# Kernel optimization log

Measured on AMD Instinct MI355X. Metric: run time of the kernel, lower is better.

The kernel has to match this reference:

```python
import jax, jax.numpy as jnp
import numpy as np

EMBED = 1024  # scale uses channel (= embed_size), faithful to original


def setup_inputs() -> dict:
    key = jax.random.key(0)
    k1, k2, k3, k4 = jax.random.split(key, 4)
    B, S, E, H = 4, 4096, EMBED, 64
    x = jax.random.normal(k1, (B, S, E), dtype=jnp.float32)
    Wk = jax.random.normal(k2, (E, H), dtype=jnp.float32) * (E ** -0.5)
    Wq = jax.random.normal(k3, (E, H), dtype=jnp.float32) * (E ** -0.5)
    Wv = jax.random.normal(k4, (E, H), dtype=jnp.float32) * (E ** -0.5)
    return {"x": x, "Wk": Wk, "Wq": Wq, "Wv": Wv}


def reference(x, Wk, Wq, Wv):
    # x: [B,S,E]; Wk/Wq/Wv: [E,H]
    B, S, E = x.shape
    k = jnp.einsum('bse,eh->bsh', x, Wk)
    q = jnp.einsum('bse,eh->bsh', x, Wq)
    v = jnp.einsum('bse,eh->bsh', x, Wv)
    # NOTE: original scales by channel**-0.5 (embed dim), not head_size
    scores = jnp.einsum('bqh,bkh->bqk', q, k) * (E ** -0.5)
    causal = jnp.tril(jnp.ones((S, S), dtype=bool))
    scores = jnp.where(causal, scores, -jnp.inf)
    attn = jax.nn.softmax(scores, axis=-1)
    # dropout treated as identity (eval mode) for deterministic reference
    out = jnp.einsum('bqk,bkh->bqh', attn, v)
    return out
```

## Files before the change

### kernel.cpp

```cpp
#include <hip/hip_runtime.h>
#include <hip/hip_bf16.h>
#include <math.h>

#define BATCH 4
#define SEQ   4096
#define EMB   1024
#define HD    64
#define SCALE 0.03125f
#define NSTRIPE 4

typedef __attribute__((ext_vector_type(8))) short short8;
typedef __attribute__((ext_vector_type(4))) float f32x4;

__device__ __forceinline__ short8 ld8g(const __hip_bfloat16* p) {
    union { uint4 u; short8 s; } cv;
    cv.u = *(const uint4*)p;
    return cv.s;
}
__device__ __forceinline__ short8 ld8l(const void* p) {
    union { uint4 u; short8 s; } cv;
    cv.u = *(const uint4*)p;
    return cv.s;
}
__device__ __forceinline__ unsigned short bfb(float a) {
    union { __hip_bfloat16 h; unsigned short u; } cv;
    cv.h = __hip_bfloat16(a);
    return cv.u;
}

__device__ __forceinline__ void gld16(const void* g, const void* lds_base) {
    __builtin_amdgcn_global_load_lds(
        (const __attribute__((address_space(1))) void*)(unsigned long long)(uintptr_t)g,
        (__attribute__((address_space(3))) void*)(unsigned)(uintptr_t)lds_base,
        16, 0, 0);
}

__global__ __launch_bounds__(256) void prep_w(
    const float* __restrict__ Wk, const float* __restrict__ Wq,
    const float* __restrict__ Wv, __hip_bfloat16* __restrict__ WT)
{
    __shared__ float ls[64][65];
    const int wsel = blockIdx.x >> 4;
    const int kblk = blockIdx.x & 15;
    const int k0   = kblk * 64;
    const float* W = (wsel == 0) ? Wq : (wsel == 1) ? Wk : Wv;
    const int t = threadIdx.x;
#pragma unroll
    for (int i = 0; i < 4; ++i) {
        const int idx = t + i * 256;
        const int row = idx >> 4;
        const int c4  = idx & 15;
        const float4 v = *(const float4*)(W + (size_t)(k0 + row) * HD + c4 * 4);
        ls[row][c4 * 4 + 0] = v.x; ls[row][c4 * 4 + 1] = v.y;
        ls[row][c4 * 4 + 2] = v.z; ls[row][c4 * 4 + 3] = v.w;
    }
    __syncthreads();
    const int h   = t >> 2;
    const int kk0 = (t & 3) * 16;
#pragma unroll
    for (int i = 0; i < 2; ++i) {
        const int kk = kk0 + i * 8;
        union { unsigned short u[8]; uint4 q; } pk;
#pragma unroll
        for (int j = 0; j < 8; ++j) pk.u[j] = bfb(ls[kk + j][h]);
        *(uint4*)(WT + (size_t)(wsel * 64 + h) * EMB + k0 + kk) = pk.q;
    }
}

__global__ __launch_bounds__(256) void gemm_proj(
    const float* __restrict__ x,
    const __hip_bfloat16* __restrict__ WT,
    __hip_bfloat16* __restrict__ qs,
    __hip_bfloat16* __restrict__ kb,
    __hip_bfloat16* __restrict__ vT)
{
    __shared__ __align__(16) char sm[8 * 1040 + 24 * 1040];
    char* smA = sm;
    char* smB = sm + 8 * 1040;

    const int tid  = threadIdx.x;
    const int lane = tid & 63;
    const int c    = lane & 15;
    const int quad = lane >> 4;
    const int w    = tid >> 6;
    const int rw   = w & 1;
    const int nh   = w >> 1;
    const int R0   = blockIdx.x * 32;

    const int rrA = lane >> 4;
    const int ciA = (lane & 15) ^ (rrA << 1);
    const int rrB = lane >> 3;
    const int ciB = (lane & 7) ^ rrB;

    const int rA  = rw * 16 + c;
    const int gA  = rA >> 2;
    const int rrr = rA & 3;
    const char* paBase = smA + gA * 1040 + rrr * 256;

    f32x4 acc[6];
#pragma unroll
    for (int f = 0; f < 6; ++f) acc[f] = (f32x4){0.f, 0.f, 0.f, 0.f};

    for (int s = 0; s < 16; ++s) {
        const int k0 = s * 64;
#pragma unroll
        for (int j = 0; j < 2; ++j) {
            const int g = w * 2 + j;
            const float* ga = x + (size_t)(R0 + g * 4 + rrA) * EMB + k0 + ciA * 4;
            gld16(ga, smA + g * 1040);
        }
#pragma unroll
        for (int j = 0; j < 6; ++j) {
            const int gb = w * 6 + j;
            const __hip_bfloat16* gw = WT + (size_t)(gb * 8 + rrB) * EMB + k0 + ciB * 8;
            gld16(gw, smB + gb * 1040);
        }
        __syncthreads();

#pragma unroll
        for (int ks = 0; ks < 2; ++ks) {
            const int ci0 = ks * 8 + quad * 2;
            const int ps0 = ci0 ^ (rrr << 1);
            const char* pa = paBase + ps0 * 16;
            const float4 fa = *(const float4*)pa;
            const float4 fb = *(const float4*)(pa + 16);
            union { unsigned short u[8]; short8 s8; } av;
            av.u[0] = bfb(fa.x); av.u[1] = bfb(fa.y);
            av.u[2] = bfb(fa.z); av.u[3] = bfb(fa.w);
            av.u[4] = bfb(fb.x); av.u[5] = bfb(fb.y);
            av.u[6] = bfb(fb.z); av.u[7] = bfb(fb.w);
#pragma unroll
            for (int f = 0; f < 6; ++f) {
                const int n   = nh * 96 + f * 16 + c;
                const int gB  = n >> 3;
                const int rB  = n & 7;
                const int psb = (ks * 4 + quad) ^ rB;
                const short8 bfrag = ld8l(smB + gB * 1040 + rB * 128 + psb * 16);
                acc[f] = __builtin_amdgcn_mfma_f32_16x16x32_bf16(av.s8, bfrag, acc[f], 0, 0, 0);
            }
        }
        __syncthreads();
    }

#pragma unroll
    for (int f = 0; f < 6; ++f) {
#pragma unroll
        for (int r = 0; r < 4; ++r) {
            const int m = R0 + rw * 16 + quad * 4 + r;
            const int n = nh * 96 + f * 16 + c;
            const float val = acc[f][r];
            if (n < 64) {
                qs[(size_t)m * HD + n] = __hip_bfloat16(val * SCALE);
            } else if (n < 128) {
                kb[(size_t)m * HD + (n - 64)] = __hip_bfloat16(val);
            } else {
                const int b  = m >> 12;
                const int sq = m & (SEQ - 1);
                const int sp = (sq & ~63) | ((sq & 15) << 2) | ((sq >> 4) & 3);
                vT[((size_t)b * HD + (n - 128)) * SEQ + sp] = __hip_bfloat16(val);
            }
        }
    }
}

__global__ __launch_bounds__(256) void attn_kernel(
    const __hip_bfloat16* __restrict__ qs,
    const __hip_bfloat16* __restrict__ kmat,
    const __hip_bfloat16* __restrict__ vT,
    float* __restrict__ outacc,
    float* __restrict__ lacc)
{
    __shared__ __align__(16) char smK[64 * 128];
    __shared__ __align__(16) char smV[64 * 128];
    __shared__ unsigned int Ps[4][16 * 36];

    const int tid  = threadIdx.x;
    const int w    = tid >> 6;
    const int lane = tid & 63;
    const int c    = lane & 15;
    const int quad = lane >> 4;

    const int g      = blockIdx.x;
    const int gen    = g >> 8;
    const int jj     = g & 255;
    const int b      = jj & 3;
    const int r_     = jj >> 2;
    const int t      = (gen & 1) ? r_ : 63 - r_;
    const int stripe = gen;
    const int q0w    = t * 64 + w * 16;

    const __hip_bfloat16* kbb = kmat + (size_t)b * SEQ * HD;
    const __hip_bfloat16* vTb = vT + (size_t)b * HD * SEQ;

    const __hip_bfloat16* qp = qs + ((size_t)b * SEQ + q0w + c) * HD + quad * 8;
    const short8 aq0 = ld8g(qp);
    const short8 aq1 = ld8g(qp + 32);

    const int rr = lane >> 3;
    const int ci = (lane & 7) ^ rr;

    f32x4 o0 = {0.f,0.f,0.f,0.f}, o1 = o0, o2 = o0, o3 = o0;
    f32x4 lp = {0.f,0.f,0.f,0.f};
    const f32x4 z = {0.f,0.f,0.f,0.f};

    for (int T = stripe; T <= t; T += NSTRIPE) {
        const int k0 = T << 6;

#pragma unroll
        for (int j = 0; j < 2; ++j) {
            const int grp = w * 2 + j;
            const int row = grp * 8 + rr;
            gld16(kbb + (size_t)(k0 + row) * HD + ci * 8, smK + grp * 1024);
            gld16(vTb + (size_t)row * SEQ + k0 + ci * 8, smV + grp * 1024);
        }
        __syncthreads();

        f32x4 sf[4];
#pragma unroll
        for (int f = 0; f < 4; ++f) {
            const int kr = f * 16 + c;
            const char* kp = smK + kr * 128;
            const short8 bk0 = ld8l(kp + ((quad    ) ^ (kr & 7)) * 16);
            const short8 bk1 = ld8l(kp + ((quad + 4) ^ (kr & 7)) * 16);
            sf[f] = __builtin_amdgcn_mfma_f32_16x16x32_bf16(aq0, bk0, z, 0, 0, 0);
            sf[f] = __builtin_amdgcn_mfma_f32_16x16x32_bf16(aq1, bk1, sf[f], 0, 0, 0);
        }

        if (T == t) {
#pragma unroll
            for (int f = 0; f < 4; ++f) {
                const int key = k0 + f * 16 + c;
#pragma unroll
                for (int r = 0; r < 4; ++r)
                    if (key > q0w + quad * 4 + r) sf[f][r] = -1e30f;
            }
        }

        float p[4][4];
#pragma unroll
        for (int f = 0; f < 4; ++f)
#pragma unroll
            for (int r = 0; r < 4; ++r)
                p[f][r] = __expf(sf[f][r]);
#pragma unroll
        for (int r = 0; r < 4; ++r) {
            lp[r] += (p[0][r] + p[1][r]) + (p[2][r] + p[3][r]);
            uint2 dd;
            dd.x = (unsigned int)bfb(p[0][r]) | ((unsigned int)bfb(p[1][r]) << 16);
            dd.y = (unsigned int)bfb(p[2][r]) | ((unsigned int)bfb(p[3][r]) << 16);
            *(uint2*)&Ps[w][(quad * 4 + r) * 36 + c * 2] = dd;
        }

        const short8 ap0 = ld8l(&Ps[w][c * 36 + quad * 4]);
        const short8 ap1 = ld8l(&Ps[w][c * 36 + 16 + quad * 4]);

        {
            const int vr = 0 * 16 + c;
            const char* vp = smV + vr * 128;
            const short8 bv0 = ld8l(vp + ((quad    ) ^ (vr & 7)) * 16);
            const short8 bv1 = ld8l(vp + ((quad + 4) ^ (vr & 7)) * 16);
            o0 = __builtin_amdgcn_mfma_f32_16x16x32_bf16(ap0, bv0, o0, 0, 0, 0);
            o0 = __builtin_amdgcn_mfma_f32_16x16x32_bf16(ap1, bv1, o0, 0, 0, 0);
        }
        {
            const int vr = 1 * 16 + c;
            const char* vp = smV + vr * 128;
            const short8 bv0 = ld8l(vp + ((quad    ) ^ (vr & 7)) * 16);
            const short8 bv1 = ld8l(vp + ((quad + 4) ^ (vr & 7)) * 16);
            o1 = __builtin_amdgcn_mfma_f32_16x16x32_bf16(ap0, bv0, o1, 0, 0, 0);
            o1 = __builtin_amdgcn_mfma_f32_16x16x32_bf16(ap1, bv1, o1, 0, 0, 0);
        }
        {
            const int vr = 2 * 16 + c;
            const char* vp = smV + vr * 128;
            const short8 bv0 = ld8l(vp + ((quad    ) ^ (vr & 7)) * 16);
            const short8 bv1 = ld8l(vp + ((quad + 4) ^ (vr & 7)) * 16);
            o2 = __builtin_amdgcn_mfma_f32_16x16x32_bf16(ap0, bv0, o2, 0, 0, 0);
            o2 = __builtin_amdgcn_mfma_f32_16x16x32_bf16(ap1, bv1, o2, 0, 0, 0);
        }
        {
            const int vr = 3 * 16 + c;
            const char* vp = smV + vr * 128;
            const short8 bv0 = ld8l(vp + ((quad    ) ^ (vr & 7)) * 16);
            const short8 bv1 = ld8l(vp + ((quad + 4) ^ (vr & 7)) * 16);
            o3 = __builtin_amdgcn_mfma_f32_16x16x32_bf16(ap0, bv0, o3, 0, 0, 0);
            o3 = __builtin_amdgcn_mfma_f32_16x16x32_bf16(ap1, bv1, o3, 0, 0, 0);
        }
        __syncthreads();
    }

#pragma unroll
    for (int r = 0; r < 4; ++r) {
        float v = lp[r];
        v += __shfl_xor(v, 1, 64);
        v += __shfl_xor(v, 2, 64);
        v += __shfl_xor(v, 4, 64);
        v += __shfl_xor(v, 8, 64);
        lp[r] = v;
    }

    float* ob = outacc + ((size_t)b * SEQ + q0w) * HD;
#pragma unroll
    for (int r = 0; r < 4; ++r) {
        const int row = quad * 4 + r;
        atomicAdd(&ob[row * HD +  0 + c], o0[r]);
        atomicAdd(&ob[row * HD + 16 + c], o1[r]);
        atomicAdd(&ob[row * HD + 32 + c], o2[r]);
        atomicAdd(&ob[row * HD + 48 + c], o3[r]);
        if (c == 0) atomicAdd(&lacc[(size_t)b * SEQ + q0w + row], lp[r]);
    }
}

__global__ __launch_bounds__(256) void normalize_kernel(
    float* __restrict__ out, const float* __restrict__ lacc)
{
    const int idx = blockIdx.x * 256 + threadIdx.x;
    out[idx] /= lacc[idx >> 6];
}

extern "C" void kernel_launch(void* const* d_in, const int* in_sizes, int n_in,
                              void* d_out, int out_size, void* d_ws, size_t ws_size,
                              hipStream_t stream)
{
    (void)in_sizes; (void)n_in; (void)out_size; (void)ws_size;
    const float* x  = (const float*)d_in[0];
    const float* Wk = (const float*)d_in[1];
    const float* Wq = (const float*)d_in[2];
    const float* Wv = (const float*)d_in[3];
    float* out = (float*)d_out;

    const size_t BSH = (size_t)BATCH * SEQ * HD;
    __hip_bfloat16* qs = (__hip_bfloat16*)d_ws;
    __hip_bfloat16* kb = qs + BSH;
    __hip_bfloat16* vT = kb + BSH;
    __hip_bfloat16* WT = vT + BSH;
    float* lacc = (float*)(WT + 192 * EMB);

    prep_w<<<48, 256, 0, stream>>>(Wk, Wq, Wv, WT);
    gemm_proj<<<BATCH * SEQ / 32, 256, 0, stream>>>(x, WT, qs, kb, vT);
    hipMemsetAsync(out, 0, BSH * sizeof(float), stream);
    hipMemsetAsync(lacc, 0, (size_t)BATCH * SEQ * sizeof(float), stream);
    attn_kernel<<<NSTRIPE * BATCH * (SEQ / 64), 256, 0, stream>>>(qs, kb, vT, out, lacc);
    normalize_kernel<<<BATCH * SEQ * HD / 256, 256, 0, stream>>>(out, lacc);
}
```

Baseline: 148.2 us.

## Double-buffer projection GEMM and replace atomic split-K reduction with partial buffers

The projection GEMM now uses two shared-memory stages so the next K-tile's global-to-LDS loads are issued before computing the current tile, with one barrier per iteration. The attention kernel writes per-stripe partial outputs and row sums to separate workspace slices instead of using float atomics. A vectorized normalize kernel then sums the stripes and divides, which removes the two memsets. This trades atomic traffic and the memsets for more workspace and extra reads in the normalize pass, and doubles the GEMM's LDS footprint.

```diff
diff --git a/kernel.cpp b/kernel.cpp
--- a/kernel.cpp
+++ b/kernel.cpp
@@ -74,9 +74,7 @@
     __hip_bfloat16* __restrict__ kb,
     __hip_bfloat16* __restrict__ vT)
 {
-    __shared__ __align__(16) char sm[8 * 1040 + 24 * 1040];
-    char* smA = sm;
-    char* smB = sm + 8 * 1040;
+    __shared__ __align__(16) char sm[2][8 * 1040 + 24 * 1040];
 
     const int tid  = threadIdx.x;
     const int lane = tid & 63;
@@ -95,28 +93,39 @@
     const int rA  = rw * 16 + c;
     const int gA  = rA >> 2;
     const int rrr = rA & 3;
-    const char* paBase = smA + gA * 1040 + rrr * 256;
 
     f32x4 acc[6];
 #pragma unroll
     for (int f = 0; f < 6; ++f) acc[f] = (f32x4){0.f, 0.f, 0.f, 0.f};
 
+#define STAGE(buf, kk)                                                          \
+    do {                                                                        \
+        char* sA = sm[buf];                                                     \
+        char* sB = sm[buf] + 8 * 1040;                                          \
+        _Pragma("unroll")                                                       \
+        for (int j = 0; j < 2; ++j) {                                           \
+            const int g = w * 2 + j;                                            \
+            gld16(x + (size_t)(R0 + g * 4 + rrA) * EMB + (kk) + ciA * 4,        \
+                  sA + g * 1040);                                               \
+        }                                                                       \
+        _Pragma("unroll")                                                       \
+        for (int j = 0; j < 6; ++j) {                                           \
+            const int gb = w * 6 + j;                                           \
+            gld16(WT + (size_t)(gb * 8 + rrB) * EMB + (kk) + ciB * 8,           \
+                  sB + gb * 1040);                                              \
+        }                                                                       \
+    } while (0)
+
+    STAGE(0, 0);
+    __syncthreads();
+
     for (int s = 0; s < 16; ++s) {
-        const int k0 = s * 64;
-#pragma unroll
-        for (int j = 0; j < 2; ++j) {
-            const int g = w * 2 + j;
-            const float* ga = x + (size_t)(R0 + g * 4 + rrA) * EMB + k0 + ciA * 4;
-            gld16(ga, smA + g * 1040);
-        }
-#pragma unroll
-        for (int j = 0; j < 6; ++j) {
-            const int gb = w * 6 + j;
-            const __hip_bfloat16* gw = WT + (size_t)(gb * 8 + rrB) * EMB + k0 + ciB * 8;
-            gld16(gw, smB + gb * 1040);
-        }
-        __syncthreads();
-
+        const int cur = s & 1, nxt = cur ^ 1;
+        if (s < 15) STAGE(nxt, (s + 1) * 64);
+
+        const char* smA = sm[cur];
+        const char* smB = sm[cur] + 8 * 1040;
+        const char* paBase = smA + gA * 1040 + rrr * 256;
 #pragma unroll
         for (int ks = 0; ks < 2; ++ks) {
             const int ci0 = ks * 8 + quad * 2;
@@ -141,6 +150,7 @@
         }
         __syncthreads();
     }
+#undef STAGE
 
 #pragma unroll
     for (int f = 0; f < 6; ++f) {
@@ -167,8 +177,8 @@
     const __hip_bfloat16* __restrict__ qs,
     const __hip_bfloat16* __restrict__ kmat,
     const __hip_bfloat16* __restrict__ vT,
-    float* __restrict__ outacc,
-    float* __restrict__ lacc)
+    float* __restrict__ Opart,
+    float* __restrict__ Lpart)
 {
     __shared__ __align__(16) char smK[64 * 128];
     __shared__ __align__(16) char smV[64 * 128];
@@ -254,37 +264,15 @@
         const short8 ap0 = ld8l(&Ps[w][c * 36 + quad * 4]);
         const short8 ap1 = ld8l(&Ps[w][c * 36 + 16 + quad * 4]);
 
-        {
-            const int vr = 0 * 16 + c;
+#pragma unroll
+        for (int f = 0; f < 4; ++f) {
+            const int vr = f * 16 + c;
             const char* vp = smV + vr * 128;
             const short8 bv0 = ld8l(vp + ((quad    ) ^ (vr & 7)) * 16);
             const short8 bv1 = ld8l(vp + ((quad + 4) ^ (vr & 7)) * 16);
-            o0 = __builtin_amdgcn_mfma_f32_16x16x32_bf16(ap0, bv0, o0, 0, 0, 0);
-            o0 = __builtin_amdgcn_mfma_f32_16x16x32_bf16(ap1, bv1, o0, 0, 0, 0);
-        }
-        {
-            const int vr = 1 * 16 + c;
-            const char* vp = smV + vr * 128;
-            const short8 bv0 = ld8l(vp + ((quad    ) ^ (vr & 7)) * 16);
-            const short8 bv1 = ld8l(vp + ((quad + 4) ^ (vr & 7)) * 16);
-            o1 = __builtin_amdgcn_mfma_f32_16x16x32_bf16(ap0, bv0, o1, 0, 0, 0);
-            o1 = __builtin_amdgcn_mfma_f32_16x16x32_bf16(ap1, bv1, o1, 0, 0, 0);
-        }
-        {
-            const int vr = 2 * 16 + c;
-            const char* vp = smV + vr * 128;
-            const short8 bv0 = ld8l(vp + ((quad    ) ^ (vr & 7)) * 16);
-            const short8 bv1 = ld8l(vp + ((quad + 4) ^ (vr & 7)) * 16);
-            o2 = __builtin_amdgcn_mfma_f32_16x16x32_bf16(ap0, bv0, o2, 0, 0, 0);
-            o2 = __builtin_amdgcn_mfma_f32_16x16x32_bf16(ap1, bv1, o2, 0, 0, 0);
-        }
-        {
-            const int vr = 3 * 16 + c;
-            const char* vp = smV + vr * 128;
-            const short8 bv0 = ld8l(vp + ((quad    ) ^ (vr & 7)) * 16);
-            const short8 bv1 = ld8l(vp + ((quad + 4) ^ (vr & 7)) * 16);
-            o3 = __builtin_amdgcn_mfma_f32_16x16x32_bf16(ap0, bv0, o3, 0, 0, 0);
-            o3 = __builtin_amdgcn_mfma_f32_16x16x32_bf16(ap1, bv1, o3, 0, 0, 0);
+            f32x4* po = (f == 0) ? &o0 : (f == 1) ? &o1 : (f == 2) ? &o2 : &o3;
+            *po = __builtin_amdgcn_mfma_f32_16x16x32_bf16(ap0, bv0, *po, 0, 0, 0);
+            *po = __builtin_amdgcn_mfma_f32_16x16x32_bf16(ap1, bv1, *po, 0, 0, 0);
         }
         __syncthreads();
     }
@@ -299,23 +287,39 @@
         lp[r] = v;
     }
 
-    float* ob = outacc + ((size_t)b * SEQ + q0w) * HD;
+    float* ob = Opart + (size_t)stripe * (BATCH * SEQ * HD)
+                      + ((size_t)b * SEQ + q0w) * HD;
 #pragma unroll
     for (int r = 0; r < 4; ++r) {
         const int row = quad * 4 + r;
-        atomicAdd(&ob[row * HD +  0 + c], o0[r]);
-        atomicAdd(&ob[row * HD + 16 + c], o1[r]);
-        atomicAdd(&ob[row * HD + 32 + c], o2[r]);
-        atomicAdd(&ob[row * HD + 48 + c], o3[r]);
-        if (c == 0) atomicAdd(&lacc[(size_t)b * SEQ + q0w + row], lp[r]);
+        ob[row * HD +  0 + c] = o0[r];
+        ob[row * HD + 16 + c] = o1[r];
+        ob[row * HD + 32 + c] = o2[r];
+        ob[row * HD + 48 + c] = o3[r];
+        if (c == 0)
+            Lpart[(size_t)stripe * (BATCH * SEQ) + (size_t)b * SEQ + q0w + row] = lp[r];
     }
 }
 
 __global__ __launch_bounds__(256) void normalize_kernel(
-    float* __restrict__ out, const float* __restrict__ lacc)
-{
-    const int idx = blockIdx.x * 256 + threadIdx.x;
-    out[idx] /= lacc[idx >> 6];
+    float* __restrict__ out,
+    const float* __restrict__ Opart,
+    const float* __restrict__ Lpart)
+{
+    const int idx4 = blockIdx.x * 256 + threadIdx.x;
+    const int row  = idx4 >> 4;
+    const float4* O4 = (const float4*)Opart;
+    float4 s = O4[idx4];
+    float  l = Lpart[row];
+#pragma unroll
+    for (int st = 1; st < NSTRIPE; ++st) {
+        const float4 v = O4[(size_t)st * (BATCH * SEQ * HD / 4) + idx4];
+        s.x += v.x; s.y += v.y; s.z += v.z; s.w += v.w;
+        l += Lpart[(size_t)st * (BATCH * SEQ) + row];
+    }
+    const float inv = 1.0f / l;
+    float4 o; o.x = s.x * inv; o.y = s.y * inv; o.z = s.z * inv; o.w = s.w * inv;
+    ((float4*)out)[idx4] = o;
 }
 
 extern "C" void kernel_launch(void* const* d_in, const int* in_sizes, int n_in,
@@ -334,12 +338,11 @@
     __hip_bfloat16* kb = qs + BSH;
     __hip_bfloat16* vT = kb + BSH;
     __hip_bfloat16* WT = vT + BSH;
-    float* lacc = (float*)(WT + 192 * EMB);
+    float* Opart = (float*)(WT + 192 * EMB);
+    float* Lpart = Opart + (size_t)NSTRIPE * BSH;
 
     prep_w<<<48, 256, 0, stream>>>(Wk, Wq, Wv, WT);
     gemm_proj<<<BATCH * SEQ / 32, 256, 0, stream>>>(x, WT, qs, kb, vT);
-    hipMemsetAsync(out, 0, BSH * sizeof(float), stream);
-    hipMemsetAsync(lacc, 0, (size_t)BATCH * SEQ * sizeof(float), stream);
-    attn_kernel<<<NSTRIPE * BATCH * (SEQ / 64), 256, 0, stream>>>(qs, kb, vT, out, lacc);
-    normalize_kernel<<<BATCH * SEQ * HD / 256, 256, 0, stream>>>(out, lacc);
-}
+    attn_kernel<<<NSTRIPE * BATCH * (SEQ / 64), 256, 0, stream>>>(qs, kb, vT, Opart, Lpart);
+    normalize_kernel<<<BATCH * SEQ * HD / 4 / 256, 256, 0, stream>>>(out, Opart, Lpart);
+}
```

Result: faster. 144.6 us (-2.4%).
